# Kernel optimization log

Hardware: AMD Instinct MI355X
Metric: run time of the kernel (lower is better)

## Reference

```python
import jax, jax.numpy as jnp
import numpy as np

GAMMA = 0.1
TAU = 0.01
N, M, K = 256, 512, 512


def setup_inputs() -> dict:
    key = jax.random.key(0)
    ks = jax.random.split(key, 10)
    nn2 = N * N
    return {
        "I": jax.random.normal(ks[0], (K, 1), dtype=jnp.float32),
        "x": jax.random.normal(ks[1], (N, 1), dtype=jnp.float32),
        "W": jax.random.normal(ks[2], (N, N), dtype=jnp.float32),
        "z": jax.random.normal(ks[3], (M, 1), dtype=jnp.float32),
        "C": jax.random.normal(ks[4], (nn2,), dtype=jnp.float32) / np.float32(np.sqrt(nn2)),
        "D": jax.random.normal(ks[5], (nn2, M), dtype=jnp.float32) / np.float32(np.sqrt(nn2)),
        "F": jax.random.normal(ks[6], (M,), dtype=jnp.float32) / np.float32(np.sqrt(M)),
        "H": jax.random.normal(ks[7], (M, nn2), dtype=jnp.float32) / np.float32(np.sqrt(M)),
        "W_in_1": jax.random.uniform(ks[8], (N, K), dtype=jnp.float32, minval=-1.0 / np.sqrt(K), maxval=1.0 / np.sqrt(K)),
        "W_in_2": jax.random.uniform(ks[9], (M, K), dtype=jnp.float32, minval=-1.0 / np.sqrt(K), maxval=1.0 / np.sqrt(K)),
    }


def reference(I, x, W, z, C, D, F, H, W_in_1, W_in_2):
    n = x.shape[0]
    # neuron state update: x' = (1-g)x + g*W@phi(x) + W_in_1@I
    phi_x = jax.nn.sigmoid(x)                       # (n,1)
    x_new = (1.0 - GAMMA) * x + GAMMA * (W @ phi_x) + W_in_1 @ I
    # Phi(x') = vec(phi(x') phi(x')^T), row-major -> (n*n, 1)
    phi_xn = jax.nn.sigmoid(x_new)                  # (n,1)
    Phi = (phi_xn * phi_xn.T).reshape(-1, 1)        # (n*n,1) outer product
    psi_z = jnp.tanh(z)                             # (m,1)
    # diag(C)@Phi is an elementwise multiply; D@psi(z) is the big GEMV
    W_new = (1.0 - GAMMA) * W + GAMMA * (C[:, None] * Phi + D @ psi_z).reshape(n, n)
    # astrocyte update: diag(F)@psi(z) elementwise; H@Phi big GEMV
    z_new = (1.0 - GAMMA * TAU) * z + GAMMA * TAU * (
        F[:, None] * psi_z + H @ Phi + W_in_2 @ I
    )
    return (x_new, W_new, z_new)
```

## Files before the change

kernel.cpp:

```cpp
#include <hip/hip_runtime.h>
#include <math.h>

#define GAMMA 0.1f
#define TAU   0.01f
#define NN    256
#define MM    512
#define KK    512

__device__ __forceinline__ float sigmoidf(float v) {
    return 1.0f / (1.0f + __expf(-v));
}
__device__ __forceinline__ float dot4(float4 a, float4 b) {
    return a.x * b.x + a.y * b.y + a.z * b.z + a.w * b.w;
}

__global__ __launch_bounds__(256) void k_state(
    const float* __restrict__ I, const float* __restrict__ x,
    const float* __restrict__ W, const float* __restrict__ z,
    const float* __restrict__ Win1,
    float* __restrict__ out, float* __restrict__ ws)
{
    const int b = blockIdx.x, t = threadIdx.x;
    if (b < 4) {
        const int wave = t >> 6, lane = t & 63;
        float4 xv = ((const float4*)x)[lane];
        float4 ph = make_float4(sigmoidf(xv.x), sigmoidf(xv.y),
                                sigmoidf(xv.z), sigmoidf(xv.w));
        float4 i0 = ((const float4*)I)[lane];
        float4 i1 = ((const float4*)I)[64 + lane];
        const int row0 = b * 64 + wave * 16;
        for (int r = 0; r < 16; ++r) {
            const int row = row0 + r;
            float4 wv = ((const float4*)(W + row * NN))[lane];
            float4 a0 = ((const float4*)(Win1 + row * KK))[lane];
            float4 a1 = ((const float4*)(Win1 + row * KK))[64 + lane];
            float acc = GAMMA * dot4(wv, ph) + dot4(a0, i0) + dot4(a1, i1);
#pragma unroll
            for (int m = 32; m; m >>= 1) acc += __shfl_xor(acc, m, 64);
            if (lane == 0) {
                float xn = (1.0f - GAMMA) * x[row] + acc;
                out[row] = xn;
                ws[row] = sigmoidf(xn);
            }
        }
    } else {
        const int idx = (b - 4) * 256 + t;
        ws[NN + idx] = tanhf(z[idx]);
    }
}

__global__ __launch_bounds__(256) void k_big(
    const float* __restrict__ W, const float* __restrict__ Cv,
    const float* __restrict__ D, const float* __restrict__ F,
    const float* __restrict__ H, const float* __restrict__ Win2,
    const float* __restrict__ I, const float* __restrict__ z,
    const float* __restrict__ ws, float* __restrict__ out)
{
    __shared__ float sm[768];
    __shared__ float red[4];
    const int b = blockIdx.x, t = threadIdx.x;

    if (b < MM) {
        if (t < 64) ((float4*)sm)[t] = ((const float4*)ws)[t];
        __syncthreads();
        const float4* H4 = (const float4*)(H + (size_t)b * (NN * NN));
        const float4 pj = ((const float4*)sm)[t & 63];
        const int wv4 = t >> 6;
        float acc = 0.0f;
#pragma unroll 8
        for (int q = 0; q < 64; ++q) {
            float4 h = H4[t + 256 * q];
            float pi = sm[wv4 + 4 * q];
            acc += pi * dot4(h, pj);
        }
        acc += Win2[(size_t)b * KK + t] * I[t]
             + Win2[(size_t)b * KK + 256 + t] * I[256 + t];
#pragma unroll
        for (int m = 32; m; m >>= 1) acc += __shfl_xor(acc, m, 64);
        if ((t & 63) == 0) red[t >> 6] = acc;
        __syncthreads();
        if (t == 0) {
            const float gt = GAMMA * TAU;
            float tot = red[0] + red[1] + red[2] + red[3];
            float ps = ws[NN + b];
            float zn = (1.0f - gt) * z[b] + gt * (F[b] * ps + tot);
            out[NN + NN * NN + b] = zn;
        }
    } else {
        if (t < 128)      ((float4*)sm)[t] = ((const float4*)(ws + NN))[t];
        else if (t < 192) ((float4*)sm)[t] = ((const float4*)ws)[t - 128];
        __syncthreads();
        const int wave = t >> 6, lane = t & 63;
        const float4 z0 = ((const float4*)sm)[lane];
        const float4 z1 = ((const float4*)sm)[64 + lane];
        const int rowbase = (b - MM) * 16 + wave * 4;
        for (int r = 0; r < 4; ++r) {
            const int row = rowbase + r;
            const float4* D4 = (const float4*)(D + (size_t)row * MM);
            float acc = dot4(D4[lane], z0) + dot4(D4[64 + lane], z1);
#pragma unroll
            for (int m = 32; m; m >>= 1) acc += __shfl_xor(acc, m, 64);
            if (lane == 0) {
                float Phi = sm[512 + (row >> 8)] * sm[512 + (row & 255)];
                float wn = (1.0f - GAMMA) * W[row]
                         + GAMMA * (Cv[row] * Phi + acc);
                out[NN + row] = wn;
            }
        }
    }
}

extern "C" void kernel_launch(void* const* d_in, const int* in_sizes, int n_in,
                              void* d_out, int out_size, void* d_ws, size_t ws_size,
                              hipStream_t stream) {
    const float* I    = (const float*)d_in[0];
    const float* x    = (const float*)d_in[1];
    const float* W    = (const float*)d_in[2];
    const float* z    = (const float*)d_in[3];
    const float* C    = (const float*)d_in[4];
    const float* D    = (const float*)d_in[5];
    const float* F    = (const float*)d_in[6];
    const float* H    = (const float*)d_in[7];
    const float* Win1 = (const float*)d_in[8];
    const float* Win2 = (const float*)d_in[9];
    float* out = (float*)d_out;
    float* ws  = (float*)d_ws;

    hipLaunchKernelGGL(k_state, dim3(6), dim3(256), 0, stream,
                       I, x, W, z, Win1, out, ws);
    hipLaunchKernelGGL(k_big, dim3(MM + (NN * NN) / 16), dim3(256), 0, stream,
                       W, C, D, F, H, Win2, I, z, ws, out);
}
```

Baseline: 315.1 us.

## Batch row loads per wave and widen grids for state and D GEMV

The state kernel moves from 4 blocks with 16 serial rows per wave to 16 blocks with 4 rows per wave, issuing all row loads up front and reducing them with interleaved shuffles. The D GEMV blocks now handle 32 rows each (8 per wave), loading every row before reducing and writing W_new as vectorized float4 stores. In the H branch the Win2 contribution is computed before the barrier and the loop unroll is raised to 16. The aim is more memory-level parallelism and fewer dependent load-reduce chains, at the cost of higher register pressure.

New measurement: 297.0 us. 1.06x faster.

```diff
diff --git a/kernel.cpp b/kernel.cpp
--- a/kernel.cpp
+++ b/kernel.cpp
@@ -10,6 +10,9 @@
 __device__ __forceinline__ float sigmoidf(float v) {
     return 1.0f / (1.0f + __expf(-v));
 }
+__device__ __forceinline__ float4 sigmoid4(float4 v) {
+    return make_float4(sigmoidf(v.x), sigmoidf(v.y), sigmoidf(v.z), sigmoidf(v.w));
+}
 __device__ __forceinline__ float dot4(float4 a, float4 b) {
     return a.x * b.x + a.y * b.y + a.z * b.z + a.w * b.w;
 }
@@ -21,30 +24,44 @@
     float* __restrict__ out, float* __restrict__ ws)
 {
     const int b = blockIdx.x, t = threadIdx.x;
-    if (b < 4) {
+    if (b < 16) {
         const int wave = t >> 6, lane = t & 63;
+        const int row0 = b * 16 + wave * 4;
         float4 xv = ((const float4*)x)[lane];
-        float4 ph = make_float4(sigmoidf(xv.x), sigmoidf(xv.y),
-                                sigmoidf(xv.z), sigmoidf(xv.w));
         float4 i0 = ((const float4*)I)[lane];
         float4 i1 = ((const float4*)I)[64 + lane];
-        const int row0 = b * 64 + wave * 16;
-        for (int r = 0; r < 16; ++r) {
-            const int row = row0 + r;
-            float4 wv = ((const float4*)(W + row * NN))[lane];
-            float4 a0 = ((const float4*)(Win1 + row * KK))[lane];
-            float4 a1 = ((const float4*)(Win1 + row * KK))[64 + lane];
-            float acc = GAMMA * dot4(wv, ph) + dot4(a0, i0) + dot4(a1, i1);
+        const float4* Wr = (const float4*)(W + row0 * NN);
+        float4 w0 = Wr[lane], w1 = Wr[lane + 64], w2 = Wr[lane + 128], w3 = Wr[lane + 192];
+        const float4* A = (const float4*)(Win1 + row0 * KK);
+        float4 a0 = A[lane],       c0 = A[lane + 64];
+        float4 a1 = A[lane + 128], c1 = A[lane + 192];
+        float4 a2 = A[lane + 256], c2 = A[lane + 320];
+        float4 a3 = A[lane + 384], c3 = A[lane + 448];
+        float4 xo = ((const float4*)x)[row0 >> 2];
+
+        float4 ph = sigmoid4(xv);
+        float s0 = GAMMA * dot4(w0, ph) + dot4(a0, i0) + dot4(c0, i1);
+        float s1 = GAMMA * dot4(w1, ph) + dot4(a1, i0) + dot4(c1, i1);
+        float s2 = GAMMA * dot4(w2, ph) + dot4(a2, i0) + dot4(c2, i1);
+        float s3 = GAMMA * dot4(w3, ph) + dot4(a3, i0) + dot4(c3, i1);
 #pragma unroll
-            for (int m = 32; m; m >>= 1) acc += __shfl_xor(acc, m, 64);
-            if (lane == 0) {
-                float xn = (1.0f - GAMMA) * x[row] + acc;
-                out[row] = xn;
-                ws[row] = sigmoidf(xn);
-            }
+        for (int m = 32; m; m >>= 1) {
+            s0 += __shfl_xor(s0, m, 64);
+            s1 += __shfl_xor(s1, m, 64);
+            s2 += __shfl_xor(s2, m, 64);
+            s3 += __shfl_xor(s3, m, 64);
+        }
+        if (lane == 0) {
+            float4 xn;
+            xn.x = (1.0f - GAMMA) * xo.x + s0;
+            xn.y = (1.0f - GAMMA) * xo.y + s1;
+            xn.z = (1.0f - GAMMA) * xo.z + s2;
+            xn.w = (1.0f - GAMMA) * xo.w + s3;
+            ((float4*)out)[row0 >> 2] = xn;
+            ((float4*)ws)[row0 >> 2] = sigmoid4(xn);
         }
     } else {
-        const int idx = (b - 4) * 256 + t;
+        const int idx = (b - 16) * 256 + t;
         ws[NN + idx] = tanhf(z[idx]);
     }
 }
@@ -62,19 +79,18 @@
 
     if (b < MM) {
         if (t < 64) ((float4*)sm)[t] = ((const float4*)ws)[t];
+        float wi = Win2[(size_t)b * KK + t] * I[t]
+                 + Win2[(size_t)b * KK + 256 + t] * I[256 + t];
         __syncthreads();
         const float4* H4 = (const float4*)(H + (size_t)b * (NN * NN));
         const float4 pj = ((const float4*)sm)[t & 63];
         const int wv4 = t >> 6;
-        float acc = 0.0f;
-#pragma unroll 8
+        float acc = wi;
+#pragma unroll 16
         for (int q = 0; q < 64; ++q) {
             float4 h = H4[t + 256 * q];
-            float pi = sm[wv4 + 4 * q];
-            acc += pi * dot4(h, pj);
+            acc += sm[wv4 + 4 * q] * dot4(h, pj);
         }
-        acc += Win2[(size_t)b * KK + t] * I[t]
-             + Win2[(size_t)b * KK + 256 + t] * I[256 + t];
 #pragma unroll
         for (int m = 32; m; m >>= 1) acc += __shfl_xor(acc, m, 64);
         if ((t & 63) == 0) red[t >> 6] = acc;
@@ -82,8 +98,7 @@
         if (t == 0) {
             const float gt = GAMMA * TAU;
             float tot = red[0] + red[1] + red[2] + red[3];
-            float ps = ws[NN + b];
-            float zn = (1.0f - gt) * z[b] + gt * (F[b] * ps + tot);
+            float zn = (1.0f - gt) * z[b] + gt * (F[b] * ws[NN + b] + tot);
             out[NN + NN * NN + b] = zn;
         }
     } else {
@@ -93,19 +108,53 @@
         const int wave = t >> 6, lane = t & 63;
         const float4 z0 = ((const float4*)sm)[lane];
         const float4 z1 = ((const float4*)sm)[64 + lane];
-        const int rowbase = (b - MM) * 16 + wave * 4;
-        for (int r = 0; r < 4; ++r) {
-            const int row = rowbase + r;
-            const float4* D4 = (const float4*)(D + (size_t)row * MM);
-            float acc = dot4(D4[lane], z0) + dot4(D4[64 + lane], z1);
+        const int row0 = (b - MM) * 32 + wave * 8;
+        const float4* R = (const float4*)(D + (size_t)row0 * MM);
+        float4 pA = R[lane],       qA = R[lane + 64];
+        float4 pB = R[lane + 128], qB = R[lane + 192];
+        float4 pC = R[lane + 256], qC = R[lane + 320];
+        float4 pD = R[lane + 384], qD = R[lane + 448];
+        float4 pE = R[lane + 512], qE = R[lane + 576];
+        float4 pF = R[lane + 640], qF = R[lane + 704];
+        float4 pG = R[lane + 768], qG = R[lane + 832];
+        float4 pH = R[lane + 896], qH = R[lane + 960];
+        float4 w0 = ((const float4*)W)[row0 >> 2],  w1 = ((const float4*)W)[(row0 >> 2) + 1];
+        float4 c0 = ((const float4*)Cv)[row0 >> 2], c1 = ((const float4*)Cv)[(row0 >> 2) + 1];
+
+        float s0 = dot4(pA, z0) + dot4(qA, z1);
+        float s1 = dot4(pB, z0) + dot4(qB, z1);
+        float s2 = dot4(pC, z0) + dot4(qC, z1);
+        float s3 = dot4(pD, z0) + dot4(qD, z1);
+        float s4 = dot4(pE, z0) + dot4(qE, z1);
+        float s5 = dot4(pF, z0) + dot4(qF, z1);
+        float s6 = dot4(pG, z0) + dot4(qG, z1);
+        float s7 = dot4(pH, z0) + dot4(qH, z1);
 #pragma unroll
-            for (int m = 32; m; m >>= 1) acc += __shfl_xor(acc, m, 64);
-            if (lane == 0) {
-                float Phi = sm[512 + (row >> 8)] * sm[512 + (row & 255)];
-                float wn = (1.0f - GAMMA) * W[row]
-                         + GAMMA * (Cv[row] * Phi + acc);
-                out[NN + row] = wn;
-            }
+        for (int m = 32; m; m >>= 1) {
+            s0 += __shfl_xor(s0, m, 64);
+            s1 += __shfl_xor(s1, m, 64);
+            s2 += __shfl_xor(s2, m, 64);
+            s3 += __shfl_xor(s3, m, 64);
+            s4 += __shfl_xor(s4, m, 64);
+            s5 += __shfl_xor(s5, m, 64);
+            s6 += __shfl_xor(s6, m, 64);
+            s7 += __shfl_xor(s7, m, 64);
+        }
+        if (lane == 0) {
+            const float phi_i = sm[512 + (row0 >> 8)];
+            const float4* PJ = (const float4*)(sm + 512);
+            float4 pj0 = PJ[(row0 & 255) >> 2], pj1 = PJ[((row0 & 255) >> 2) + 1];
+            float4 r0, r1;
+            r0.x = (1.0f - GAMMA) * w0.x + GAMMA * (c0.x * phi_i * pj0.x + s0);
+            r0.y = (1.0f - GAMMA) * w0.y + GAMMA * (c0.y * phi_i * pj0.y + s1);
+            r0.z = (1.0f - GAMMA) * w0.z + GAMMA * (c0.z * phi_i * pj0.z + s2);
+            r0.w = (1.0f - GAMMA) * w0.w + GAMMA * (c0.w * phi_i * pj0.w + s3);
+            r1.x = (1.0f - GAMMA) * w1.x + GAMMA * (c1.x * phi_i * pj1.x + s4);
+            r1.y = (1.0f - GAMMA) * w1.y + GAMMA * (c1.y * phi_i * pj1.y + s5);
+            r1.z = (1.0f - GAMMA) * w1.z + GAMMA * (c1.z * phi_i * pj1.z + s6);
+            r1.w = (1.0f - GAMMA) * w1.w + GAMMA * (c1.w * phi_i * pj1.w + s7);
+            ((float4*)(out + NN + row0))[0] = r0;
+            ((float4*)(out + NN + row0))[1] = r1;
         }
     }
 }
@@ -126,8 +175,8 @@
     float* out = (float*)d_out;
     float* ws  = (float*)d_ws;
 
-    hipLaunchKernelGGL(k_state, dim3(6), dim3(256), 0, stream,
+    hipLaunchKernelGGL(k_state, dim3(18), dim3(256), 0, stream,
                        I, x, W, z, Win1, out, ws);
-    hipLaunchKernelGGL(k_big, dim3(MM + (NN * NN) / 16), dim3(256), 0, stream,
+    hipLaunchKernelGGL(k_big, dim3(MM + (NN * NN) / 32), dim3(256), 0, stream,
                        W, C, D, F, H, Win2, I, z, ws, out);
 }
```
